# Kernel tuning notes

Measured on AMD Instinct MI355X. Metric: run time of the kernel, lower is better.

The kernel has to match this reference:

```python
import jax, jax.numpy as jnp
import numpy as np

N_P, E_P = 50000, 400000
N_L, E_L = 50000, 400000
B = 256  # number of graphs per side
NEG_GAT = 0.2   # GATv2 leaky-relu slope
NEG_FC = 0.01   # nn.LeakyReLU default slope


def _gatv2(x, ei, Wl, Wr, att, b, H, C):
    """GATv2Conv (concat heads, add_self_loops=True). Wl/Wr: [in, H*C], att: [H, C], b: [H*C]."""
    N = x.shape[0]
    sl = jnp.arange(N)
    src = jnp.concatenate([ei[0], sl])
    dst = jnp.concatenate([ei[1], sl])
    xl = (x @ Wl).reshape(N, H, C)   # source transform (messages)
    xr = (x @ Wr).reshape(N, H, C)   # target transform
    e = jax.nn.leaky_relu(xl[src] + xr[dst], NEG_GAT)          # [E+N, H, C]
    logits = jnp.einsum('ehc,hc->eh', e, att)                   # [E+N, H]
    m = jax.ops.segment_max(logits, dst, num_segments=N)        # segment softmax
    a = jnp.exp(logits - m[dst])
    alpha = a / jax.ops.segment_sum(a, dst, num_segments=N)[dst]
    out = jax.ops.segment_sum(xl[src] * alpha[..., None], dst, num_segments=N)
    return out.reshape(N, H * C) + b


def _mean_pool(x, batch, nb):
    s = jax.ops.segment_sum(x, batch, num_segments=nb)
    c = jax.ops.segment_sum(jnp.ones((x.shape[0],), x.dtype), batch, num_segments=nb)
    return s / jnp.maximum(c, 1.0)[:, None]


def setup_inputs() -> dict:
    key = jax.random.key(0)
    ks = jax.random.split(key, 48)
    i = [0]
    def nrm(shape, fan_in):
        k = ks[i[0]]; i[0] += 1
        return jax.random.normal(k, shape, jnp.float32) / np.sqrt(fan_in)
    inp = {}
    inp['protein_x'] = jax.random.normal(ks[40], (N_P, 10), jnp.float32)
    inp['ligand_x'] = jax.random.normal(ks[41], (N_L, 5), jnp.float32)
    inp['protein_edge_index'] = jax.random.randint(ks[42], (2, E_P), 0, N_P)
    inp['ligand_edge_index'] = jax.random.randint(ks[43], (2, E_L), 0, N_L)
    inp['protein_batch'] = (jnp.arange(N_P) * B) // N_P  # sorted graph ids, all segments nonempty
    inp['ligand_batch'] = (jnp.arange(N_L) * B) // N_L
    # GATv2 params: layer1 heads=2 out=128, layer2 heads=1 out=256
    inp['p1_Wl'] = nrm((10, 256), 10); inp['p1_Wr'] = nrm((10, 256), 10)
    inp['p1_att'] = nrm((2, 128), 128); inp['p1_b'] = jnp.zeros((256,), jnp.float32)
    inp['p2_Wl'] = nrm((256, 256), 256); inp['p2_Wr'] = nrm((256, 256), 256)
    inp['p2_att'] = nrm((1, 256), 256); inp['p2_b'] = jnp.zeros((256,), jnp.float32)
    inp['l1_Wl'] = nrm((5, 256), 5); inp['l1_Wr'] = nrm((5, 256), 5)
    inp['l1_att'] = nrm((2, 128), 128); inp['l1_b'] = jnp.zeros((256,), jnp.float32)
    inp['l2_Wl'] = nrm((256, 256), 256); inp['l2_Wr'] = nrm((256, 256), 256)
    inp['l2_att'] = nrm((1, 256), 256); inp['l2_b'] = jnp.zeros((256,), jnp.float32)
    # MultiheadAttention(256, 4) params ([in, out] convention)
    inp['Wq'] = nrm((256, 256), 256); inp['bq'] = jnp.zeros((256,), jnp.float32)
    inp['Wk'] = nrm((256, 256), 256); inp['bk'] = jnp.zeros((256,), jnp.float32)
    inp['Wv'] = nrm((256, 256), 256); inp['bv'] = jnp.zeros((256,), jnp.float32)
    inp['Wo'] = nrm((256, 256), 256); inp['bo'] = jnp.zeros((256,), jnp.float32)
    # fc head
    inp['fc1_w'] = nrm((512, 256), 512); inp['fc1_b'] = jnp.zeros((256,), jnp.float32)
    inp['ln_g'] = jnp.ones((256,), jnp.float32); inp['ln_b'] = jnp.zeros((256,), jnp.float32)
    inp['fc2_w'] = nrm((256, 1), 256); inp['fc2_b'] = jnp.zeros((1,), jnp.float32)
    return inp


def reference(protein_x, protein_edge_index, protein_batch,
              ligand_x, ligand_edge_index, ligand_batch,
              p1_Wl, p1_Wr, p1_att, p1_b, p2_Wl, p2_Wr, p2_att, p2_b,
              l1_Wl, l1_Wr, l1_att, l1_b, l2_Wl, l2_Wr, l2_att, l2_b,
              Wq, bq, Wk, bk, Wv, bv, Wo, bo,
              fc1_w, fc1_b, ln_g, ln_b, fc2_w, fc2_b):
    px = _gatv2(protein_x, protein_edge_index, p1_Wl, p1_Wr, p1_att, p1_b, 2, 128)
    px = _gatv2(px, protein_edge_index, p2_Wl, p2_Wr, p2_att, p2_b, 1, 256)
    px = _mean_pool(px, protein_batch, B)                        # [B, 256]
    lx = _gatv2(ligand_x, ligand_edge_index, l1_Wl, l1_Wr, l1_att, l1_b, 2, 128)
    lx = _gatv2(lx, ligand_edge_index, l2_Wl, l2_Wr, l2_att, l2_b, 1, 256)
    lx = _mean_pool(lx, ligand_batch, B)                         # [B, 256]
    # cross attention with q/k/v seq length 1
    D, H = 256, 4
    d = D // H
    qh = (px @ Wq + bq).reshape(B, H, d)
    kh = (lx @ Wk + bk).reshape(B, H, d)
    vh = (lx @ Wv + bv).reshape(B, H, d)
    scores = (qh * kh).sum(-1) / jnp.sqrt(jnp.float32(d))        # [B, H], 1 key
    w = jax.nn.softmax(scores[..., None], axis=-1)               # all ones (single key)
    attn = (w * vh).reshape(B, D) @ Wo + bo                      # [B, 256]
    comb = jnp.concatenate([px, attn], axis=1)                   # [B, 512]
    h = comb @ fc1_w + fc1_b
    mu = h.mean(-1, keepdims=True)
    var = h.var(-1, keepdims=True)
    h = (h - mu) / jnp.sqrt(var + 1e-5) * ln_g + ln_b
    h = jax.nn.leaky_relu(h, NEG_FC)
    return h @ fc2_w + fc2_b                                     # [B, 1]
```

## Files before the change

### kernel.cpp

```cpp
#include <hip/hip_runtime.h>
#include <math.h>

typedef unsigned short u16;
typedef __attribute__((ext_vector_type(8))) short bf16x8;
typedef __attribute__((ext_vector_type(4))) float f32x4;

#define LOG2E 1.4426950408889634f

__device__ inline u16 f2bf(float x) {
  unsigned int u = __float_as_uint(x);
  u += 0x7fffu + ((u >> 16) & 1u);
  return (u16)(u >> 16);
}
__device__ inline float bf2f(u16 h) {
  return __uint_as_float(((unsigned int)h) << 16);
}
__device__ inline float4 ld_bf4(const u16* p) {
  ushort4 v = *(const ushort4*)p;
  return make_float4(bf2f(v.x), bf2f(v.y), bf2f(v.z), bf2f(v.w));
}

__global__ void k_setup(int* __restrict__ cnt, int nz,
                        const float* __restrict__ W2pl, const float* __restrict__ W2pr,
                        const float* __restrict__ W2ll, const float* __restrict__ W2lr,
                        u16* __restrict__ Whp, u16* __restrict__ Wlp,
                        u16* __restrict__ Whl, u16* __restrict__ Wll_o,
                        const float* __restrict__ xp, int Kp, int Np,
                        const float* __restrict__ xl_, int Kl, int Nl,
                        const float* __restrict__ W1pl, const float* __restrict__ W1pr,
                        const float* __restrict__ W1ll, const float* __restrict__ W1lr,
                        u16* __restrict__ xlh_p, u16* __restrict__ xrh_p,
                        u16* __restrict__ xlh_l, u16* __restrict__ xrh_l,
                        int linPer,
                        const float* __restrict__ Wo, const float* __restrict__ fc1w_,
                        float* __restrict__ Wof) {
  __shared__ float xs[16][8];
  __shared__ float sW[256];
  const int zb = (nz + 255) / 256;
  if ((int)blockIdx.x < zb) {
    int i = blockIdx.x * 256 + threadIdx.x;
    if (i < nz) cnt[i] = 0;
    return;
  }
  int wb = blockIdx.x - zb;
  if (wb < 1024) {
    int n = wb & 511;
    int side = wb >> 9;
    int col = n & 255;
    int k = threadIdx.x;
    const float* W = side == 0 ? (n < 256 ? W2pl : W2pr) : (n < 256 ? W2ll : W2lr);
    float w = W[k * 256 + col];
    u16* Wh = side ? Whl : Whp;
    u16* Wlo = side ? Wll_o : Wlp;
    u16 hb = f2bf(w);
    Wh[n * 256 + k] = hb;
    Wlo[n * 256 + k] = f2bf(w - bf2f(hb));
    return;
  }
  int wb2 = wb - 1024;
  if (wb2 >= 2 * linPer) {
    int row = wb2 - 2 * linPer;
    if (row >= 256) return;
    int jj = threadIdx.x;
    sW[jj] = Wo[row * 256 + jj];
    __syncthreads();
    float a0 = 0.f, a1 = 0.f, a2 = 0.f, a3 = 0.f;
    for (int c = 0; c < 256; c += 4) {
      a0 = fmaf(sW[c], fc1w_[(256 + c) * 256 + jj], a0);
      a1 = fmaf(sW[c + 1], fc1w_[(256 + c + 1) * 256 + jj], a1);
      a2 = fmaf(sW[c + 2], fc1w_[(256 + c + 2) * 256 + jj], a2);
      a3 = fmaf(sW[c + 3], fc1w_[(256 + c + 3) * 256 + jj], a3);
    }
    Wof[row * 256 + jj] = (a0 + a1) + (a2 + a3);
    return;
  }
  const int side = wb2 / linPer;
  const float* x = side ? xl_ : xp;
  const int K = side ? Kl : Kp;
  const int N = side ? Nl : Np;
  const float* Wl = side ? W1ll : W1pl;
  const float* Wr = side ? W1lr : W1pr;
  u16* xlh = side ? xlh_l : xlh_p;
  u16* xrh = side ? xrh_l : xrh_p;
  int base = (wb2 - side * linPer) * 8;
  if (base >= N) return;
  int j = threadIdx.x;
  int tot = 8 * K;
  for (int i = j; i < tot; i += 256) {
    int r = i / K, k = i - r * K;
    if (base + r < N) xs[k][r] = x[(size_t)(base + r) * K + k];
  }
  __syncthreads();
  float al[8] = {}, ar[8] = {};
  for (int k = 0; k < K; ++k) {
    float wl = Wl[k * 256 + j];
    float wr = Wr[k * 256 + j];
#pragma unroll
    for (int r = 0; r < 8; ++r) {
      al[r] = fmaf(xs[k][r], wl, al[r]);
      ar[r] = fmaf(xs[k][r], wr, ar[r]);
    }
  }
#pragma unroll
  for (int r = 0; r < 8; ++r) {
    int n = base + r;
    if (n < N) {
      xlh[(size_t)n * 256 + j] = f2bf(al[r]);
      xrh[(size_t)n * 256 + j] = f2bf(ar[r]);
    }
  }
}

__global__ void k_histb(const int* __restrict__ eip, int Ep, const int* __restrict__ eil,
                        int El, int* __restrict__ cntp, int* __restrict__ cntl,
                        int histB,
                        const float* __restrict__ Wv, const float* __restrict__ Wof,
                        const float* __restrict__ fc1w_, const float* __restrict__ bv,
                        const float* __restrict__ bo, const float* __restrict__ fc1b,
                        float* __restrict__ W2, float* __restrict__ biasEff) {
  __shared__ float sV[256];
  if ((int)blockIdx.x >= histB) {
    int g2 = blockIdx.x - histB;
    int jj = threadIdx.x;
    if (g2 < 256) {
      sV[jj] = Wv[g2 * 256 + jj];
      __syncthreads();
      float a0 = 0.f, a1 = 0.f, a2 = 0.f, a3 = 0.f;
      for (int m = 0; m < 256; m += 4) {
        a0 = fmaf(sV[m], Wof[m * 256 + jj], a0);
        a1 = fmaf(sV[m + 1], Wof[(m + 1) * 256 + jj], a1);
        a2 = fmaf(sV[m + 2], Wof[(m + 2) * 256 + jj], a2);
        a3 = fmaf(sV[m + 3], Wof[(m + 3) * 256 + jj], a3);
      }
      W2[g2 * 256 + jj] = (a0 + a1) + (a2 + a3);
    } else {
      float acc = fc1b[jj];
      for (int k = 0; k < 256; ++k) acc = fmaf(bv[k], Wof[k * 256 + jj], acc);
      for (int k = 0; k < 256; ++k) acc = fmaf(bo[k], fc1w_[(256 + k) * 256 + jj], acc);
      biasEff[jj] = acc;
    }
    return;
  }
  int e = blockIdx.x * blockDim.x + threadIdx.x;
  if (e < Ep) atomicAdd(&cntp[eip[Ep + e]], 1);
  else if (e < Ep + El) { int e2 = e - Ep; atomicAdd(&cntl[eil[El + e2]], 1); }
}

__global__ void k_scan1b(const int* __restrict__ cntp, int Np, const int* __restrict__ cntl,
                         int Nl, int nbp, int* __restrict__ offsp, int* __restrict__ offsl,
                         int* __restrict__ curp, int* __restrict__ curl,
                         int* __restrict__ bsum) {
  __shared__ int s[256];
  int tid = threadIdx.x;
  int side = ((int)blockIdx.x >= nbp) ? 1 : 0;
  int blk = side ? (blockIdx.x - nbp) : blockIdx.x;
  const int* cnt = side ? cntl : cntp;
  int* offs = side ? offsl : offsp;
  int* cur = side ? curl : curp;
  int N = side ? Nl : Np;
  int i = blk * 256 + tid;
  int v = (i < N) ? cnt[i] : 0;
  if (i < N) cur[i] = 0;
  s[tid] = v;
  __syncthreads();
  for (int off = 1; off < 256; off <<= 1) {
    int t = 0;
    if (tid >= off) t = s[tid - off];
    __syncthreads();
    if (tid >= off) s[tid] += t;
    __syncthreads();
  }
  if (i < N) offs[i] = s[tid] - v;
  if (tid == 255) bsum[side * 256 + blk] = s[255];
}

__global__ void k_scan2b(int* __restrict__ bsum, int nbp, int nbl) {
  __shared__ int s[256];
  int side = blockIdx.x;
  int nb = side ? nbl : nbp;
  int* bs = bsum + side * 256;
  int tid = threadIdx.x;
  int v = (tid < nb) ? bs[tid] : 0;
  s[tid] = v;
  __syncthreads();
  for (int off = 1; off < 256; off <<= 1) {
    int t = 0;
    if (tid >= off) t = s[tid - off];
    __syncthreads();
    if (tid >= off) s[tid] += t;
    __syncthreads();
  }
  if (tid < nb) bs[tid] = s[tid] - v;
}

__global__ void k_fillb(const int* __restrict__ eip, int Ep, const int* __restrict__ eil,
                        int El, const int* __restrict__ offsp, const int* __restrict__ offsl,
                        const int* __restrict__ bsum,
                        int* __restrict__ curp, int* __restrict__ curl,
                        int* __restrict__ csrp, int* __restrict__ csrl) {
  int e = blockIdx.x * blockDim.x + threadIdx.x;
  if (e < Ep) {
    int d = eip[Ep + e];
    int pos = offsp[d] + bsum[d >> 8] + atomicAdd(&curp[d], 1);
    csrp[pos] = eip[e];
  } else if (e < Ep + El) {
    int e2 = e - Ep;
    int d = eil[El + e2];
    int pos = offsl[d] + bsum[256 + (d >> 8)] + atomicAdd(&curl[d], 1);
    csrl[pos] = eil[e2];
  }
}

__global__ void __launch_bounds__(256, 2) k_mm_dual_b(
    const u16* __restrict__ A_p, const u16* __restrict__ A_l,
    const u16* __restrict__ Bh_p, const u16* __restrict__ Bl_p,
    const u16* __restrict__ Bh_l, const u16* __restrict__ Bl_l,
    u16* __restrict__ XLh_p, u16* __restrict__ XRh_p,
    u16* __restrict__ XLh_l, u16* __restrict__ XRh_l, int Np, int Nl, int Rp, int Rtot) {
  __shared__ __align__(16) char smem[32768];
  char* sA = smem;
  char* sBh = smem + 8192;
  char* sBl = smem + 16384;
  const int gid = blockIdx.x;
  const int rblk = (gid >> 5) * 8 + (gid & 7);
  const int col = (gid >> 3) & 3;
  if (rblk >= Rtot) return;
  const int side = (rblk >= Rp) ? 1 : 0;
  const int rloc = side ? rblk - Rp : rblk;
  const u16* A = side ? A_l : A_p;
  const u16* Bhi = side ? Bh_l : Bh_p;
  const u16* Blo = side ? Bl_l : Bl_p;
  u16* XLh = side ? XLh_l : XLh_p;
  u16* XRh = side ? XRh_l : XRh_p;
  const int M = side ? Nl : Np;
  const int t = threadIdx.x;
  const int rowBase = rloc * 128;
  const int j0 = col * 128;
  const int srow = t >> 1;
  const int h = t & 1;
  int gr = rowBase + srow;
  if (gr >= M) gr = M - 1;
  const size_t gaBase = (size_t)gr * 256 + h * 16;
  const size_t gbBase = (size_t)(j0 + srow) * 256 + h * 16;
  const int rb = srow * 64;
  const int sw0 = (((h * 2) + (srow >> 1)) & 3) * 16;
  const int sw1 = (((h * 2 + 1) + (srow >> 1)) & 3) * 16;
  const int lane = t & 63;
  const int wid = t >> 6;
  const int wm = (wid & 1) * 64;
  const int wn = (wid >> 1) * 64;
  const int kq = lane >> 4;
  const int mr = lane & 15;
  int offA[4], offB[4];
#pragma unroll
  for (int i = 0; i < 4; ++i) {
    int m = wm + i * 16 + mr;
    offA[i] = m * 64 + ((kq + (m >> 1)) & 3) * 16;
    int n = wn + i * 16 + mr;
    offB[i] = n * 64 + ((kq + (n >> 1)) & 3) * 16;
  }
  f32x4 acc[4][4] = {};
  uint4 va0 = *(const uint4*)(A + gaBase);
  uint4 va1 = *(const uint4*)(A + gaBase + 8);
  uint4 vbh0 = *(const uint4*)(Bhi + gbBase);
  uint4 vbh1 = *(const uint4*)(Bhi + gbBase + 8);
  uint4 vbl0 = *(const uint4*)(Blo + gbBase);
  uint4 vbl1 = *(const uint4*)(Blo + gbBase + 8);
#pragma unroll
  for (int kt = 0; kt < 8; ++kt) {
    __syncthreads();
    *(uint4*)(sA + rb + sw0) = va0;
    *(uint4*)(sA + rb + sw1) = va1;
    *(uint4*)(sBh + rb + sw0) = vbh0;
    *(uint4*)(sBh + rb + sw1) = vbh1;
    *(uint4*)(sBl + rb + sw0) = vbl0;
    *(uint4*)(sBl + rb + sw1) = vbl1;
    __syncthreads();
    if (kt < 7) {
      const int k0 = (kt + 1) * 32;
      va0 = *(const uint4*)(A + gaBase + k0);
      va1 = *(const uint4*)(A + gaBase + k0 + 8);
      vbh0 = *(const uint4*)(Bhi + gbBase + k0);
      vbh1 = *(const uint4*)(Bhi + gbBase + k0 + 8);
      vbl0 = *(const uint4*)(Blo + gbBase + k0);
      vbl1 = *(const uint4*)(Blo + gbBase + k0 + 8);
    }
    bf16x8 a[4], bh[4], bl[4];
#pragma unroll
    for (int i = 0; i < 4; ++i) {
      a[i] = *(const bf16x8*)(sA + offA[i]);
      bh[i] = *(const bf16x8*)(sBh + offB[i]);
      bl[i] = *(const bf16x8*)(sBl + offB[i]);
    }
#pragma unroll
    for (int i = 0; i < 4; ++i)
#pragma unroll
      for (int j = 0; j < 4; ++j) {
        acc[i][j] = __builtin_amdgcn_mfma_f32_16x16x32_bf16(a[i], bh[j], acc[i][j], 0, 0, 0);
        acc[i][j] = __builtin_amdgcn_mfma_f32_16x16x32_bf16(a[i], bl[j], acc[i][j], 0, 0, 0);
      }
  }
  __syncthreads();
  u16* wtile = (u16*)(smem + wid * 8192);
#pragma unroll
  for (int i = 0; i < 4; ++i)
#pragma unroll
    for (int j = 0; j < 4; ++j)
#pragma unroll
      for (int r = 0; r < 4; ++r)
        wtile[(i * 16 + kq * 4 + r) * 64 + j * 16 + mr] = f2bf(acc[i][j][r]);
  u16* cbase = (col < 2) ? XLh : XRh;
  const int cb = (col < 2) ? j0 : j0 - 256;
  const int r8 = lane >> 3;
  const int c8 = lane & 7;
#pragma unroll
  for (int rr = 0; rr < 8; ++rr) {
    int lr = rr * 8 + r8;
    uint4 v = *(const uint4*)&wtile[lr * 64 + c8 * 8];
    int row = rowBase + wm + lr;
    if (row < M) *(uint4*)&cbase[(size_t)row * 256 + cb + wn + c8 * 8] = v;
  }
}

#define GAT_DOT(a, q)                                                          \
  {                                                                            \
    float t0 = a.x + rd.x, t1 = a.y + rd.y, t2 = a.z + rd.z, t3 = a.w + rd.w;  \
    q = fmaf(t3, wa6.w, fabsf(t3) * wa4.w);                                    \
    q = fmaf(fabsf(t2), wa4.z, fmaf(t2, wa6.z, q));                            \
    q = fmaf(fabsf(t1), wa4.y, fmaf(t1, wa6.y, q));                            \
    q = fmaf(fabsf(t0), wa4.x, fmaf(t0, wa6.x, q));                            \
  }

template <int H>
__global__ void k_gat_gather_b(
    const u16* __restrict__ xlh_p, const u16* __restrict__ xrh_p, u16* __restrict__ out_p,
    const u16* __restrict__ xlh_l, const u16* __restrict__ xrh_l, u16* __restrict__ out_l,
    const int* __restrict__ csr_p, const int* __restrict__ offs_p,
    const int* __restrict__ cnt_p,
    const int* __restrict__ csr_l, const int* __restrict__ offs_l,
    const int* __restrict__ cnt_l, const int* __restrict__ bsum,
    const float* __restrict__ att_p, const float* __restrict__ bias_p,
    const float* __restrict__ att_l, const float* __restrict__ bias_l,
    int Np, int Nl) {
  const int side = blockIdx.y;
  const u16* xlh = side ? xlh_l : xlh_p;
  const u16* xrh = side ? xrh_l : xrh_p;
  u16* out = side ? out_l : out_p;
  const int* csr = side ? csr_l : csr_p;
  const int* offs = side ? offs_l : offs_p;
  const int* cnt = side ? cnt_l : cnt_p;
  const float* att = side ? att_l : att_p;
  const float* bias = side ? bias_l : bias_p;
  const int N = side ? Nl : Np;
  int d = blockIdx.x * 4 + (threadIdx.x >> 6);
  if (d >= N) return;
  const int lo4 = (threadIdx.x & 63) * 4;
  const float4 rd = ld_bf4(&xrh[(size_t)d * 256 + lo4]);
  const float4 wa = *(const float4*)&att[lo4];
  const float4 wa6 = make_float4(0.6f * LOG2E * wa.x, 0.6f * LOG2E * wa.y,
                                 0.6f * LOG2E * wa.z, 0.6f * LOG2E * wa.w);
  const float4 wa4 = make_float4(0.4f * LOG2E * wa.x, 0.4f * LOG2E * wa.y,
                                 0.4f * LOG2E * wa.z, 0.4f * LOG2E * wa.w);
  const float4 xd = ld_bf4(&xlh[(size_t)d * 256 + lo4]);
  float base;
  GAT_DOT(xd, base)
#pragma unroll
  for (int off = 1; off <= (H == 2 ? 16 : 32); off <<= 1) base += __shfl_xor(base, off, 64);
  float l0 = 1.f, l1 = 0.f, l2 = 0.f, l3 = 0.f;
  float4 acc0 = xd;
  float4 acc1 = make_float4(0.f, 0.f, 0.f, 0.f);
  float4 acc2 = make_float4(0.f, 0.f, 0.f, 0.f);
  float4 acc3 = make_float4(0.f, 0.f, 0.f, 0.f);
  const int o0 = offs[d] + bsum[side * 256 + (d >> 8)];
  const int c = cnt[d];
  int j = 0;
  for (; j + 3 < c; j += 4) {
    int s0 = csr[o0 + j], s1 = csr[o0 + j + 1], s2 = csr[o0 + j + 2], s3 = csr[o0 + j + 3];
    float4 a0 = ld_bf4(&xlh[(size_t)s0 * 256 + lo4]);
    float4 a1 = ld_bf4(&xlh[(size_t)s1 * 256 + lo4]);
    float4 a2 = ld_bf4(&xlh[(size_t)s2 * 256 + lo4]);
    float4 a3 = ld_bf4(&xlh[(size_t)s3 * 256 + lo4]);
    float q0, q1, q2, q3;
    GAT_DOT(a0, q0)
    GAT_DOT(a1, q1)
    GAT_DOT(a2, q2)
    GAT_DOT(a3, q3)
#pragma unroll
    for (int off = 1; off <= (H == 2 ? 16 : 32); off <<= 1) {
      q0 += __shfl_xor(q0, off, 64);
      q1 += __shfl_xor(q1, off, 64);
      q2 += __shfl_xor(q2, off, 64);
      q3 += __shfl_xor(q3, off, 64);
    }
    float w0 = __builtin_amdgcn_exp2f(q0 - base), w1 = __builtin_amdgcn_exp2f(q1 - base);
    float w2 = __builtin_amdgcn_exp2f(q2 - base), w3 = __builtin_amdgcn_exp2f(q3 - base);
    l0 += w0; l1 += w1; l2 += w2; l3 += w3;
    acc0.x = fmaf(w0, a0.x, acc0.x); acc0.y = fmaf(w0, a0.y, acc0.y);
    acc0.z = fmaf(w0, a0.z, acc0.z); acc0.w = fmaf(w0, a0.w, acc0.w);
    acc1.x = fmaf(w1, a1.x, acc1.x); acc1.y = fmaf(w1, a1.y, acc1.y);
    acc1.z = fmaf(w1, a1.z, acc1.z); acc1.w = fmaf(w1, a1.w, acc1.w);
    acc2.x = fmaf(w2, a2.x, acc2.x); acc2.y = fmaf(w2, a2.y, acc2.y);
    acc2.z = fmaf(w2, a2.z, acc2.z); acc2.w = fmaf(w2, a2.w, acc2.w);
    acc3.x = fmaf(w3, a3.x, acc3.x); acc3.y = fmaf(w3, a3.y, acc3.y);
    acc3.z = fmaf(w3, a3.z, acc3.z); acc3.w = fmaf(w3, a3.w, acc3.w);
  }
  for (; j < c; ++j) {
    int s0 = csr[o0 + j];
    float4 a0 = ld_bf4(&xlh[(size_t)s0 * 256 + lo4]);
    float q0;
    GAT_DOT(a0, q0)
#pragma unroll
    for (int off = 1; off <= (H == 2 ? 16 : 32); off <<= 1) q0 += __shfl_xor(q0, off, 64);
    float w0 = __builtin_amdgcn_exp2f(q0 - base);
    l0 += w0;
    acc0.x = fmaf(w0, a0.x, acc0.x); acc0.y = fmaf(w0, a0.y, acc0.y);
    acc0.z = fmaf(w0, a0.z, acc0.z); acc0.w = fmaf(w0, a0.w, acc0.w);
  }
  float inv = 1.f / (l0 + l1 + l2 + l3);
  float ax = acc0.x + acc1.x + acc2.x + acc3.x;
  float ay = acc0.y + acc1.y + acc2.y + acc3.y;
  float az = acc0.z + acc1.z + acc2.z + acc3.z;
  float aw = acc0.w + acc1.w + acc2.w + acc3.w;
  const float4 b4 = *(const float4*)&bias[lo4];
  ushort4 hv;
  hv.x = f2bf(ax * inv + b4.x);
  hv.y = f2bf(ay * inv + b4.y);
  hv.z = f2bf(az * inv + b4.z);
  hv.w = f2bf(aw * inv + b4.w);
  *(ushort4*)&out[(size_t)d * 256 + lo4] = hv;
}

#define POOL_C 8
__global__ void k_pool_part(const u16* __restrict__ xp, const int* __restrict__ bp, int Np,
                            const u16* __restrict__ xl_, const int* __restrict__ bl_, int Nl,
                            float* __restrict__ PPpart, float* __restrict__ LPpart) {
  const int b = blockIdx.x;
  const int side = blockIdx.y;
  const int chunk = blockIdx.z;
  const u16* x = side ? xl_ : xp;
  const int* batch = side ? bl_ : bp;
  const int N = side ? Nl : Np;
  float* part = side ? LPpart : PPpart;
  int j = threadIdx.x;
  __shared__ int sss, sse;
  if (j == 0) {
    int lo = 0, hi = N;
    while (lo < hi) { int mid = (lo + hi) >> 1; if (batch[mid] < b) lo = mid + 1; else hi = mid; }
    sss = lo;
    lo = 0; hi = N;
    while (lo < hi) { int mid = (lo + hi) >> 1; if (batch[mid] < b + 1) lo = mid + 1; else hi = mid; }
    sse = lo;
  }
  __syncthreads();
  int len = sse - sss;
  int per = (len + POOL_C - 1) / POOL_C;
  int st = sss + chunk * per;
  int en = st + per;
  if (en > sse) en = sse;
  float acc = 0.f;
  for (int n = st; n < en; ++n) acc += bf2f(x[(size_t)n * 256 + j]);
  part[((size_t)chunk * 256 + b) * 256 + j] = acc;
}

__global__ void k_head(const float* __restrict__ PPpart, const float* __restrict__ LPpart,
                       const int* __restrict__ bp, int Np,
                       const int* __restrict__ bl_, int Nl,
                       const float* __restrict__ fc1w, const float* __restrict__ W2,
                       const float* __restrict__ biasEff,
                       const float* __restrict__ lng, const float* __restrict__ lnb,
                       const float* __restrict__ fc2w, const float* __restrict__ fc2b,
                       float* __restrict__ out) {
  int b = blockIdx.x;
  int t = threadIdx.x;
  int j = t & 255;
  __shared__ float xs0[256], xs1[256];
  __shared__ float part[2][256];
  __shared__ float r1[256], r2[256];
  __shared__ float smu, srs;
  __shared__ int seg[4];
  if (t < 2) {
    const int* batch = t ? bl_ : bp;
    int N = t ? Nl : Np;
    int lo = 0, hi = N;
    while (lo < hi) { int mid = (lo + hi) >> 1; if (batch[mid] < b) lo = mid + 1; else hi = mid; }
    seg[t * 2] = lo;
    lo = 0; hi = N;
    while (lo < hi) { int mid = (lo + hi) >> 1; if (batch[mid] < b + 1) lo = mid + 1; else hi = mid; }
    seg[t * 2 + 1] = lo;
  }
  __syncthreads();
  if (t < 256) {
    float accp = 0.f;
#pragma unroll
    for (int c = 0; c < POOL_C; ++c) accp += PPpart[((size_t)c * 256 + b) * 256 + j];
    xs0[j] = accp / fmaxf((float)(seg[1] - seg[0]), 1.f);
  } else {
    float accl = 0.f;
#pragma unroll
    for (int c = 0; c < POOL_C; ++c) accl += LPpart[((size_t)c * 256 + b) * 256 + j];
    xs1[j] = accl / fmaxf((float)(seg[3] - seg[2]), 1.f);
  }
  __syncthreads();
  {
    const float* src = (t < 256) ? xs0 : xs1;
    const float* W = (t < 256) ? fc1w : W2;
    float a0 = 0.f, a1 = 0.f, a2 = 0.f, a3 = 0.f;
    for (int k = 0; k < 256; k += 4) {
      a0 = fmaf(src[k], W[k * 256 + j], a0);
      a1 = fmaf(src[k + 1], W[(k + 1) * 256 + j], a1);
      a2 = fmaf(src[k + 2], W[(k + 2) * 256 + j], a2);
      a3 = fmaf(src[k + 3], W[(k + 3) * 256 + j], a3);
    }
    part[t >> 8][j] = (a0 + a1) + (a2 + a3);
  }
  __syncthreads();
  float h = 0.f;
  if (t < 256) {
    h = part[0][j] + part[1][j] + biasEff[j];
    r1[j] = h;
    r2[j] = h * h;
  }
  __syncthreads();
  for (int off = 128; off > 0; off >>= 1) {
    if (t < off) { r1[t] += r1[t + off]; r2[t] += r2[t + off]; }
    __syncthreads();
  }
  if (t == 0) {
    float mu = r1[0] / 256.f;
    float var = r2[0] / 256.f - mu * mu;
    smu = mu;
    srs = 1.f / sqrtf(var + 1e-5f);
  }
  __syncthreads();
  if (t < 256) {
    float hn = (h - smu) * srs * lng[j] + lnb[j];
    hn = hn > 0.f ? hn : 0.01f * hn;
    r1[j] = hn * fc2w[j];
  }
  __syncthreads();
  for (int off = 128; off > 0; off >>= 1) {
    if (t < off) r1[t] += r1[t + off];
    __syncthreads();
  }
  if (t == 0) out[b] = r1[0] + fc2b[0];
}

extern "C" void kernel_launch(void* const* d_in, const int* in_sizes, int n_in,
                              void* d_out, int out_size, void* d_ws, size_t ws_size,
                              hipStream_t stream) {
  const float* px = (const float*)d_in[0];
  const float* lx = (const float*)d_in[1];
  const int* pei = (const int*)d_in[2];
  const int* lei = (const int*)d_in[3];
  const int* pb = (const int*)d_in[4];
  const int* lb = (const int*)d_in[5];
  const float* p1_Wl = (const float*)d_in[6];
  const float* p1_Wr = (const float*)d_in[7];
  const float* p1_att = (const float*)d_in[8];
  const float* p1_b = (const float*)d_in[9];
  const float* p2_Wl = (const float*)d_in[10];
  const float* p2_Wr = (const float*)d_in[11];
  const float* p2_att = (const float*)d_in[12];
  const float* p2_b = (const float*)d_in[13];
  const float* l1_Wl = (const float*)d_in[14];
  const float* l1_Wr = (const float*)d_in[15];
  const float* l1_att = (const float*)d_in[16];
  const float* l1_b = (const float*)d_in[17];
  const float* l2_Wl = (const float*)d_in[18];
  const float* l2_Wr = (const float*)d_in[19];
  const float* l2_att = (const float*)d_in[20];
  const float* l2_b = (const float*)d_in[21];
  const float* Wv = (const float*)d_in[26];
  const float* bv = (const float*)d_in[27];
  const float* Wo = (const float*)d_in[28];
  const float* bo = (const float*)d_in[29];
  const float* fc1w = (const float*)d_in[30];
  const float* fc1b = (const float*)d_in[31];
  const float* lng = (const float*)d_in[32];
  const float* lnb = (const float*)d_in[33];
  const float* fc2w = (const float*)d_in[34];
  const float* fc2b = (const float*)d_in[35];

  const int NPn = in_sizes[4];
  const int NLn = in_sizes[5];
  const int EPe = in_sizes[2] / 2;
  const int ELe = in_sizes[3] / 2;
  const int KP = in_sizes[0] / NPn;
  const int KL = in_sizes[1] / NLn;

  const int Nmax = NPn > NLn ? NPn : NLn;
  const int Emax = EPe > ELe ? EPe : ELe;
  size_t NF = (size_t)Nmax * 256;

  u16* XLh_p = (u16*)d_ws;
  u16* XRh_p = XLh_p + NF;
  u16* Ah_p = XRh_p + NF;
  u16* XLh_l = Ah_p + NF;
  u16* XRh_l = XLh_l + NF;
  u16* Ah_l = XRh_l + NF;
  u16* Wth = Ah_l + NF;
  u16* Wtl = Wth + 2 * 512 * 256;
  float* PPpart = (float*)(Wtl + 2 * 512 * 256);
  float* LPpart = PPpart + (size_t)POOL_C * 256 * 256;
  int* cnt = (int*)(LPpart + (size_t)POOL_C * 256 * 256);
  int* cur = cnt + 2 * (size_t)Nmax;
  int* offs = cur + 2 * (size_t)Nmax;
  int* bsum = offs + 2 * (size_t)Nmax;
  int* csr = bsum + 512;
  int* cnt_l = cnt + Nmax;
  int* cur_l = cur + Nmax;
  int* offs_l = offs + Nmax;
  int* csr_l = csr + Emax;
  float* Wof = (float*)(csr + 2 * (size_t)Emax);
  float* W2f = Wof + 65536;
  float* bEff = W2f + 65536;

  const int nbp = (NPn + 255) / 256;
  const int nbl = (NLn + 255) / 256;
  const int nz = 2 * Nmax;
  const int zb = (nz + 255) / 256;
  const int linPer = (Nmax + 7) / 8;
  const int histB = (EPe + ELe + 255) / 256;

  k_setup<<<zb + 1024 + 2 * linPer + 256, 256, 0, stream>>>(
      cnt, nz, p2_Wl, p2_Wr, l2_Wl, l2_Wr,
      Wth, Wtl, Wth + 512 * 256, Wtl + 512 * 256,
      px, KP, NPn, lx, KL, NLn, p1_Wl, p1_Wr, l1_Wl, l1_Wr,
      XLh_p, XRh_p, XLh_l, XRh_l, linPer, Wo, fc1w, Wof);
  k_histb<<<histB + 257, 256, 0, stream>>>(pei, EPe, lei, ELe, cnt, cnt_l, histB,
                                           Wv, Wof, fc1w, bv, bo, fc1b, W2f, bEff);
  k_scan1b<<<nbp + nbl, 256, 0, stream>>>(cnt, NPn, cnt_l, NLn, nbp, offs, offs_l,
                                          cur, cur_l, bsum);
  k_scan2b<<<2, 256, 0, stream>>>(bsum, nbp, nbl);
  k_fillb<<<(EPe + ELe + 255) / 256, 256, 0, stream>>>(pei, EPe, lei, ELe, offs, offs_l,
                                                       bsum, cur, cur_l, csr, csr_l);
  k_gat_gather_b<2><<<dim3((Nmax + 3) / 4, 2), 256, 0, stream>>>(
      XLh_p, XRh_p, Ah_p, XLh_l, XRh_l, Ah_l,
      csr, offs, cnt, csr_l, offs_l, cnt_l, bsum,
      p1_att, p1_b, l1_att, l1_b, NPn, NLn);
  {
    const int Rp = (NPn + 127) / 128;
    const int Rl = (NLn + 127) / 128;
    const int Rtot = Rp + Rl;
    k_mm_dual_b<<<32 * ((Rtot + 7) / 8), 256, 0, stream>>>(
        Ah_p, Ah_l, Wth, Wtl, Wth + 512 * 256, Wtl + 512 * 256,
        XLh_p, XRh_p, XLh_l, XRh_l, NPn, NLn, Rp, Rtot);
  }
  k_gat_gather_b<1><<<dim3((Nmax + 3) / 4, 2), 256, 0, stream>>>(
      XLh_p, XRh_p, Ah_p, XLh_l, XRh_l, Ah_l,
      csr, offs, cnt, csr_l, offs_l, cnt_l, bsum,
      p2_att, p2_b, l2_att, l2_b, NPn, NLn);
  k_pool_part<<<dim3(256, 2, POOL_C), 256, 0, stream>>>(Ah_p, pb, NPn, Ah_l, lb, NLn,
                                                        PPpart, LPpart);
  k_head<<<256, 512, 0, stream>>>(PPpart, LPpart, pb, NPn, lb, NLn,
                                  fc1w, W2f, bEff, lng, lnb, fc2w, fc2b,
                                  (float*)d_out);
  (void)n_in; (void)out_size; (void)ws_size;
}
```

Before: 518.5 us.

## Double-buffer GEMM tiles via direct global-to-LDS loads; vectorize pooling reduction

The dual-side GEMM kernel now loads A and B tiles straight from global memory into LDS with global_load_lds, so tiles no longer pass through registers. LDS is double-buffered to 48KB so the next k-tile loads while MFMAs run on the current one. The swizzle is moved to the global address side to keep the LDS layout the same. The pooling kernel now reads 4 bf16 values per thread across 4 row groups and reduces them in shared memory. The larger LDS use may lower occupancy, and the explicit vmcnt wait plus barrier each step limits how much overlap is possible.

```diff
diff --git a/kernel.cpp b/kernel.cpp
--- a/kernel.cpp
+++ b/kernel.cpp
@@ -18,6 +18,11 @@
 __device__ inline float4 ld_bf4(const u16* p) {
   ushort4 v = *(const ushort4*)p;
   return make_float4(bf2f(v.x), bf2f(v.y), bf2f(v.z), bf2f(v.w));
+}
+__device__ inline void gload_lds16(const u16* g, char* lds) {
+  __builtin_amdgcn_global_load_lds(
+      (const __attribute__((address_space(1))) unsigned int*)g,
+      (__attribute__((address_space(3))) unsigned int*)lds, 16, 0, 0);
 }
 
 __global__ void k_setup(int* __restrict__ cnt, int nz,
@@ -217,10 +222,7 @@
     const u16* __restrict__ Bh_l, const u16* __restrict__ Bl_l,
     u16* __restrict__ XLh_p, u16* __restrict__ XRh_p,
     u16* __restrict__ XLh_l, u16* __restrict__ XRh_l, int Np, int Nl, int Rp, int Rtot) {
-  __shared__ __align__(16) char smem[32768];
-  char* sA = smem;
-  char* sBh = smem + 8192;
-  char* sBl = smem + 16384;
+  __shared__ __align__(16) char smem[49152];
   const int gid = blockIdx.x;
   const int rblk = (gid >> 5) * 8 + (gid & 7);
   const int col = (gid >> 3) & 3;
@@ -236,17 +238,23 @@
   const int t = threadIdx.x;
   const int rowBase = rloc * 128;
   const int j0 = col * 128;
-  const int srow = t >> 1;
-  const int h = t & 1;
-  int gr = rowBase + srow;
-  if (gr >= M) gr = M - 1;
-  const size_t gaBase = (size_t)gr * 256 + h * 16;
-  const size_t gbBase = (size_t)(j0 + srow) * 256 + h * 16;
-  const int rb = srow * 64;
-  const int sw0 = (((h * 2) + (srow >> 1)) & 3) * 16;
-  const int sw1 = (((h * 2 + 1) + (srow >> 1)) & 3) * 16;
   const int lane = t & 63;
   const int wid = t >> 6;
+  const int srow0 = wid * 32 + (lane >> 2);
+  const int cL = lane & 3;
+  int rA0 = rowBase + srow0;
+  if (rA0 >= M) rA0 = M - 1;
+  int rA1 = rowBase + srow0 + 16;
+  if (rA1 >= M) rA1 = M - 1;
+  const int rB0 = j0 + srow0;
+  const int rB1 = j0 + srow0 + 16;
+  const int c0 = (cL - ((srow0 >> 1) & 3)) & 3;
+  const int c1 = (cL - (((srow0 + 16) >> 1) & 3)) & 3;
+  const size_t gA0 = (size_t)rA0 * 256 + c0 * 8;
+  const size_t gA1 = (size_t)rA1 * 256 + c1 * 8;
+  const size_t gB0 = (size_t)rB0 * 256 + c0 * 8;
+  const size_t gB1 = (size_t)rB1 * 256 + c1 * 8;
+  const int seg = wid * 2048;
   const int wm = (wid & 1) * 64;
   const int wn = (wid >> 1) * 64;
   const int kq = lane >> 4;
@@ -260,37 +268,30 @@
     offB[i] = n * 64 + ((kq + (n >> 1)) & 3) * 16;
   }
   f32x4 acc[4][4] = {};
-  uint4 va0 = *(const uint4*)(A + gaBase);
-  uint4 va1 = *(const uint4*)(A + gaBase + 8);
-  uint4 vbh0 = *(const uint4*)(Bhi + gbBase);
-  uint4 vbh1 = *(const uint4*)(Bhi + gbBase + 8);
-  uint4 vbl0 = *(const uint4*)(Blo + gbBase);
-  uint4 vbl1 = *(const uint4*)(Blo + gbBase + 8);
+  auto stage = [&](int bsel, int kt) {
+    char* bb = smem + bsel * 24576;
+    const int k0 = kt * 32;
+    gload_lds16(A + gA0 + k0, bb + seg);
+    gload_lds16(A + gA1 + k0, bb + seg + 1024);
+    gload_lds16(Bhi + gB0 + k0, bb + 8192 + seg);
+    gload_lds16(Bhi + gB1 + k0, bb + 8192 + seg + 1024);
+    gload_lds16(Blo + gB0 + k0, bb + 16384 + seg);
+    gload_lds16(Blo + gB1 + k0, bb + 16384 + seg + 1024);
+  };
+  stage(0, 0);
 #pragma unroll
   for (int kt = 0; kt < 8; ++kt) {
-    __syncthreads();
-    *(uint4*)(sA + rb + sw0) = va0;
-    *(uint4*)(sA + rb + sw1) = va1;
-    *(uint4*)(sBh + rb + sw0) = vbh0;
-    *(uint4*)(sBh + rb + sw1) = vbh1;
-    *(uint4*)(sBl + rb + sw0) = vbl0;
-    *(uint4*)(sBl + rb + sw1) = vbl1;
-    __syncthreads();
-    if (kt < 7) {
-      const int k0 = (kt + 1) * 32;
-      va0 = *(const uint4*)(A + gaBase + k0);
-      va1 = *(const uint4*)(A + gaBase + k0 + 8);
-      vbh0 = *(const uint4*)(Bhi + gbBase + k0);
-      vbh1 = *(const uint4*)(Bhi + gbBase + k0 + 8);
-      vbl0 = *(const uint4*)(Blo + gbBase + k0);
-      vbl1 = *(const uint4*)(Blo + gbBase + k0 + 8);
-    }
+    const int cur = kt & 1;
+    asm volatile("s_waitcnt vmcnt(0)" ::: "memory");
+    __syncthreads();
+    if (kt < 7) stage(cur ^ 1, kt + 1);
+    const char* bb = smem + cur * 24576;
     bf16x8 a[4], bh[4], bl[4];
 #pragma unroll
     for (int i = 0; i < 4; ++i) {
-      a[i] = *(const bf16x8*)(sA + offA[i]);
-      bh[i] = *(const bf16x8*)(sBh + offB[i]);
-      bl[i] = *(const bf16x8*)(sBl + offB[i]);
+      a[i] = *(const bf16x8*)(bb + offA[i]);
+      bh[i] = *(const bf16x8*)(bb + 8192 + offB[i]);
+      bl[i] = *(const bf16x8*)(bb + 16384 + offB[i]);
     }
 #pragma unroll
     for (int i = 0; i < 4; ++i)
@@ -441,9 +442,10 @@
   const int* batch = side ? bl_ : bp;
   const int N = side ? Nl : Np;
   float* part = side ? LPpart : PPpart;
-  int j = threadIdx.x;
+  int t = threadIdx.x;
   __shared__ int sss, sse;
-  if (j == 0) {
+  __shared__ float red[4][256];
+  if (t == 0) {
     int lo = 0, hi = N;
     while (lo < hi) { int mid = (lo + hi) >> 1; if (batch[mid] < b) lo = mid + 1; else hi = mid; }
     sss = lo;
@@ -457,9 +459,20 @@
   int st = sss + chunk * per;
   int en = st + per;
   if (en > sse) en = sse;
-  float acc = 0.f;
-  for (int n = st; n < en; ++n) acc += bf2f(x[(size_t)n * 256 + j]);
-  part[((size_t)chunk * 256 + b) * 256 + j] = acc;
+  const int r = t >> 6;
+  const int lane = t & 63;
+  float4 acc = make_float4(0.f, 0.f, 0.f, 0.f);
+  for (int n = st + r; n < en; n += 4) {
+    float4 v = ld_bf4(&x[(size_t)n * 256 + lane * 4]);
+    acc.x += v.x; acc.y += v.y; acc.z += v.z; acc.w += v.w;
+  }
+  red[r][lane * 4 + 0] = acc.x;
+  red[r][lane * 4 + 1] = acc.y;
+  red[r][lane * 4 + 2] = acc.z;
+  red[r][lane * 4 + 3] = acc.w;
+  __syncthreads();
+  part[((size_t)chunk * 256 + b) * 256 + t] =
+      red[0][t] + red[1][t] + red[2][t] + red[3][t];
 }
 
 __global__ void k_head(const float* __restrict__ PPpart, const float* __restrict__ LPpart,
```

Result: faster. 503.9 us (-2.8%).
